# Kernel optimization log

Measured on AMD Instinct MI355X. Metric: run time of the kernel, lower is better.

Reference implementation:

```python
import jax, jax.numpy as jnp
import numpy as np

KS = 3          # kernel_size
DIL = 6         # dilation
PAD = 6         # padding
N = KS * KS     # sampling points per pixel
EPS = 1e-5      # BatchNorm eps


def conv2d(x, w, b=None, padding=0):
    out = jax.lax.conv_general_dilated(
        x, w, window_strides=(1, 1),
        padding=[(padding, padding), (padding, padding)],
        dimension_numbers=('NCHW', 'OIHW', 'NCHW'))
    if b is not None:
        out = out + b[None, :, None, None]
    return out


def setup_inputs() -> dict:
    key = jax.random.key(0)
    ks = jax.random.split(key, 6)
    B, C, H, W, P = 4, 256, 64, 64, 256
    x = jax.random.normal(ks[0], (B, C, H, W), jnp.float32)
    # offset-predicting conv (2N channels), kaiming-ish scale, kept small so offsets are sane
    w_p = jax.random.normal(ks[1], (2 * N, C, 3, 3), jnp.float32) * 0.02
    b_p = jnp.zeros((2 * N,), jnp.float32)
    # modulation-mask conv (N channels)
    w_m = jax.random.normal(ks[2], (N, C, 3, 3), jnp.float32) * 0.02
    b_m = jnp.zeros((N,), jnp.float32)
    # main deform-conv weight (no bias)
    w = jax.random.normal(ks[3], (P, C, KS, KS), jnp.float32) * (2.0 / (C * N)) ** 0.5
    gamma = jnp.ones((P,), jnp.float32)   # BN weight (init fill 1)
    beta = jnp.zeros((P,), jnp.float32)   # BN bias  (init fill 0)
    return dict(x=x, w_p=w_p, b_p=b_p, w_m=w_m, b_m=b_m, w=w, gamma=gamma, beta=beta)


def deform_conv(x, w_p, b_p, w_m, b_m, w):
    B, C, H, W = x.shape
    offset = conv2d(x, w_p, b_p, padding=1)                 # [B, 2N, H, W]
    m = jax.nn.sigmoid(conv2d(x, w_m, b_m, padding=1))      # [B, N, H, W] modulation mask

    x_pad = jnp.pad(x, ((0, 0), (0, 0), (PAD, PAD), (PAD, PAD)))
    Hp, Wp = H + 2 * PAD, W + 2 * PAD

    # p = p_0 (base grid, starts at 1 into padded map) + p_n (dilated kernel grid) + offset
    r = (KS - 1) // 2
    pn = jnp.arange(-r, r + 1, dtype=jnp.float32) * DIL
    pn_x, pn_y = jnp.meshgrid(pn, pn, indexing='ij')        # row-major matches conv weight layout
    p0_x = jnp.arange(1, H + 1, dtype=jnp.float32)
    p0_y = jnp.arange(1, W + 1, dtype=jnp.float32)
    off_x = offset[:, :N].transpose(0, 2, 3, 1)             # [B, H, W, N]
    off_y = offset[:, N:].transpose(0, 2, 3, 1)
    px = p0_x[None, :, None, None] + pn_x.reshape(-1)[None, None, None, :] + off_x
    py = p0_y[None, None, :, None] + pn_y.reshape(-1)[None, None, None, :] + off_y

    q_lt_x = jnp.clip(jnp.floor(px), 0, Hp - 1)
    q_lt_y = jnp.clip(jnp.floor(py), 0, Wp - 1)
    q_rb_x = jnp.clip(jnp.floor(px) + 1, 0, Hp - 1)
    q_rb_y = jnp.clip(jnp.floor(py) + 1, 0, Wp - 1)
    px = jnp.clip(px, 0, Hp - 1)
    py = jnp.clip(py, 0, Wp - 1)

    x_flat = x_pad.reshape(B, C, Hp * Wp)

    def gather(qx, qy):
        idx = (qx * Wp + qy).astype(jnp.int32).reshape(B, 1, -1)   # [B,1,H*W*N]
        v = jnp.take_along_axis(x_flat, jnp.broadcast_to(idx, (B, C, idx.shape[-1])), axis=2)
        return v.reshape(B, C, H, W, N)

    # bilinear weights (deform-conv-v2 formulation)
    g_lt = (1 + (q_lt_x - px)) * (1 + (q_lt_y - py))
    g_rb = (1 - (q_rb_x - px)) * (1 - (q_rb_y - py))
    g_lb = (1 + (q_lt_x - px)) * (1 - (q_rb_y - py))
    g_rt = (1 - (q_rb_x - px)) * (1 + (q_lt_y - py))

    x_off = (g_lt[:, None] * gather(q_lt_x, q_lt_y)
             + g_rb[:, None] * gather(q_rb_x, q_rb_y)
             + g_lb[:, None] * gather(q_lt_x, q_rb_y)
             + g_rt[:, None] * gather(q_rb_x, q_lt_y))     # [B, C, H, W, N]

    x_off = x_off * m.transpose(0, 2, 3, 1)[:, None]        # apply modulation

    # stride-KS conv over the tiled x_offset == einsum over kernel positions
    wk = w.reshape(w.shape[0], C, N)
    return jnp.einsum('bchwk,ock->bohw', x_off, wk)


def reference(x, w_p, b_p, w_m, b_m, w, gamma, beta):
    y = deform_conv(x, w_p, b_p, w_m, b_m, w)
    # BatchNorm2d, training mode (batch stats, biased variance)
    mean = y.mean(axis=(0, 2, 3), keepdims=True)
    var = ((y - mean) ** 2).mean(axis=(0, 2, 3), keepdims=True)
    y = (y - mean) * jax.lax.rsqrt(var + EPS)
    y = y * gamma[None, :, None, None] + beta[None, :, None, None]
    return jax.nn.relu(y)
```

## Files before the change

kernel.cpp:

```cpp
#include <hip/hip_runtime.h>
#include <math.h>

#define CC 256
#define PP 256
#define XSTR 296

#define WS_OFF   0ull
#define WS_Y     442368ull
#define WS_SUM   4636672ull
#define WS_SUMSQ 4636928ull
#define WS_SCALE 4637184ull
#define WS_SHIFT 4637440ull
#define WS_XT    4637696ull
#define WS_WF    6734848ull
#define WS_WPMF  7029760ull

typedef __attribute__((ext_vector_type(8))) short bf16x8;
typedef __attribute__((ext_vector_type(4))) float f32x4;

static __device__ inline unsigned short f2bf(float f) {
  unsigned int u = __float_as_uint(f);
  unsigned int r = (u + 0x7FFFu + ((u >> 16) & 1u)) >> 16;
  return (unsigned short)r;
}
static __device__ inline float bf2f(short s) {
  return __uint_as_float(((unsigned)(unsigned short)s) << 16);
}

__global__ __launch_bounds__(256) void k_prep(const float* __restrict__ x,
                                              const float* __restrict__ w,
                                              const float* __restrict__ w_p,
                                              const float* __restrict__ w_m,
                                              float* __restrict__ ws) {
  int blk = blockIdx.x, t = threadIdx.x;
  if (blk < 1024) {
    __shared__ float sT[64][65];
    int b = blk >> 8, h = (blk >> 2) & 63, c0 = (blk & 3) * 64;
    const float* xs = x + ((size_t)(b * 256 + c0) * 64 + h) * 64;
    int cl = t >> 6, wl = t & 63;
#pragma unroll
    for (int it = 0; it < 16; ++it) {
      int c = cl + it * 4;
      sT[c][wl] = xs[(size_t)c * 4096 + wl];
    }
    __syncthreads();
    unsigned short* xt = (unsigned short*)(ws + WS_XT) +
                         ((size_t)b * 64 + h) * 16384 + c0;
    int c2 = t & 63, w2l = t >> 6;
#pragma unroll
    for (int it = 0; it < 16; ++it) {
      int w2 = w2l + it * 4;
      xt[(size_t)w2 * 256 + c2] = f2bf(sT[c2][w2]);
    }
  } else {
    int gid = (blk - 1024) * 256 + t;
    if (blk == 1024 && t < 512) ws[WS_SUM + t] = 0.f;
    unsigned short* wfb = (unsigned short*)(ws + WS_WF);
    for (int e = gid; e < 589824; e += 163840) {
      int j = e & 7, ocin = (e >> 3) & 15, quad = (e >> 7) & 3;
      int ot = (e >> 9) & 15, ksg = e >> 13;
      int kb = ksg / 9, ks = ksg - kb * 9;
      int c = kb * 32 + quad * 8 + j;
      int oc = ot * 16 + ocin;
      wfb[e] = f2bf(w[((size_t)oc * CC + c) * 9 + ks]);
    }
    unsigned short* wpmf = (unsigned short*)(ws + WS_WPMF);
    for (int e = gid; e < 73728; e += 163840) {
      int j = e & 7, ocin = (e >> 3) & 15, quad = (e >> 7) & 3;
      int ot = (e >> 9) & 1, ksg = e >> 10;
      int kb = ksg / 9, ks = ksg - kb * 9;
      int c = kb * 32 + quad * 8 + j;
      int oc = ot * 16 + ocin;
      float v = 0.f;
      if (oc < 18)      v = w_p[((size_t)oc * CC + c) * 9 + ks];
      else if (oc < 27) v = w_m[((size_t)(oc - 18) * CC + c) * 9 + ks];
      wpmf[e] = f2bf(v);
    }
  }
}

__global__ __launch_bounds__(512, 4) void k_offmask(const float* __restrict__ b_p,
                                                    const float* __restrict__ b_m,
                                                    float* __restrict__ ws) {
  const unsigned short* xT = (const unsigned short*)(ws + WS_XT);
  const unsigned short* wpmf = (const unsigned short*)(ws + WS_WPMF);
  float* offm = ws + WS_OFF;
  __shared__ __align__(16) unsigned short sXo0[32 * XSTR];
  __shared__ __align__(16) unsigned short sXo1[32 * XSTR];

  int t = threadIdx.x, blk = blockIdx.x;
  int xcd = blk & 7, ii = blk >> 3;
  int b = xcd >> 1, h = (xcd & 1) * 32 + (ii >> 1), side = ii & 1;

  int lane = t & 63, wv = __builtin_amdgcn_readfirstlane(t >> 6);
  int pxt = wv & 1, ot = (wv >> 1) & 1, kh = wv >> 2;
  f32x4 acc = {0.f, 0.f, 0.f, 0.f};
  const unsigned short* xb = xT + (size_t)b * 1048576;
  int q = t & 3, uq = t >> 2;

  int oa[3], odst[3];
#pragma unroll
  for (int r = 0; r < 3; ++r) {
    int u = r * 128 + uq;
    odst[r] = -1;
    oa[r] = -1;
    if (u < 288) {
      int j = u >> 5, px = u & 31;
      int row = h + j / 3 - 1, col = side * 32 + px + j % 3 - 1;
      odst[r] = px * XSTR + j * 32 + q * 8;
      if ((unsigned)row < 64u && (unsigned)col < 64u)
        oa[r] = (row * 64 + col) * 256 + q * 8;
    }
  }

  auto stage = [&](int kb, unsigned short* buf) {
    int cb = kb * 32;
#pragma unroll
    for (int r = 0; r < 3; ++r) {
      if (odst[r] >= 0) {
        bf16x8 v = {0, 0, 0, 0, 0, 0, 0, 0};
        if (oa[r] >= 0) v = *(const bf16x8*)(xb + oa[r] + cb);
        *(bf16x8*)&buf[odst[r]] = v;
      }
    }
  };

  stage(0, sXo0);
  __syncthreads();
  for (int kb = 0; kb < 8; ++kb) {
    unsigned short* cur = (kb & 1) ? sXo1 : sXo0;
    unsigned short* nxt = (kb & 1) ? sXo0 : sXo1;
    if (kb < 7) stage(kb + 1, nxt);
    const unsigned short* bb =
        &cur[(pxt * 16 + (lane & 15)) * XSTR + (lane >> 4) * 8];
#pragma unroll
    for (int ks = 0; ks < 9; ++ks) {
      if ((int)(ks >= 5) == kh) {
        int ksg = kb * 9 + ks;
        bf16x8 af =
            *(const bf16x8*)(wpmf + (size_t)ksg * 1024 + ot * 512 + lane * 8);
        bf16x8 bf = *(const bf16x8*)(bb + ks * 32);
        acc = __builtin_amdgcn_mfma_f32_16x16x32_bf16(af, bf, acc, 0, 0, 0);
      }
    }
    __syncthreads();
  }

  float* sR = (float*)sXo0;
  if (kh == 1) {
    int base = (pxt * 2 + ot) * 256 + lane * 4;
#pragma unroll
    for (int r = 0; r < 4; ++r) sR[base + r] = acc[r];
  }
  __syncthreads();
  if (kh == 0) {
    int base = (pxt * 2 + ot) * 256 + lane * 4;
    int pxl = side * 32 + pxt * 16 + (lane & 15);
#pragma unroll
    for (int r = 0; r < 4; ++r) {
      int oc = ot * 16 + (lane >> 4) * 4 + r;
      if (oc < 27) {
        float v = acc[r] + sR[base + r];
        v += (oc < 18) ? b_p[oc] : b_m[oc - 18];
        if (oc >= 18) v = 1.f / (1.f + expf(-v));
        offm[((size_t)b * 27 + oc) * 4096 + h * 64 + pxl] = v;
      }
    }
  }
}

__global__ __launch_bounds__(512, 4) void k_deform(float* __restrict__ ws) {
  const float* offm = ws + WS_OFF;
  const unsigned short* xT = (const unsigned short*)(ws + WS_XT);
  const unsigned short* wfb = (const unsigned short*)(ws + WS_WF);
  float* y = ws + WS_Y;

  __shared__ __align__(16) unsigned short sXu0[32 * XSTR];
  __shared__ __align__(16) unsigned short sXu1[32 * XSTR];

  int t = threadIdx.x, blk = blockIdx.x;
  int xcd = blk & 7, ii = blk >> 3;
  int b = xcd >> 1, h = (xcd & 1) * 32 + (ii >> 1), side = ii & 1;

  int q = t & 3, uq = t >> 2;
  int ta0[3], ta1[3], ta2[3], ta3[3], tdst[3];
  float tg0[3], tg1[3], tg2[3], tg3[3];
#pragma unroll
  for (int r = 0; r < 3; ++r) {
    int u = r * 128 + uq;
    tdst[r] = -1;
    if (u < 288) {
      int k = u >> 5, px = u & 31;
      int w = side * 32 + px;
      size_t base = ((size_t)b * 27) * 4096 + h * 64 + w;
      float offx = offm[base + (size_t)k * 4096];
      float offy = offm[base + (size_t)(9 + k) * 4096];
      float mk   = offm[base + (size_t)(18 + k) * 4096];
      float pnx = (float)((k / 3 - 1) * 6);
      float pny = (float)((k % 3 - 1) * 6);
      float pxf = (float)(h + 1) + pnx + offx;
      float pyf = (float)(w + 1) + pny + offy;
      float fx = floorf(pxf), fy = floorf(pyf);
      float q0x = fminf(fmaxf(fx, 0.f), 75.f);
      float q1x = fminf(fmaxf(fx + 1.f, 0.f), 75.f);
      float q0y = fminf(fmaxf(fy, 0.f), 75.f);
      float q1y = fminf(fmaxf(fy + 1.f, 0.f), 75.f);
      float pxc = fminf(fmaxf(pxf, 0.f), 75.f);
      float pyc = fminf(fmaxf(pyf, 0.f), 75.f);
      float glt = (1.f + (q0x - pxc)) * (1.f + (q0y - pyc));
      float grb = (1.f - (q1x - pxc)) * (1.f - (q1y - pyc));
      float glb = (1.f + (q0x - pxc)) * (1.f - (q1y - pyc));
      float grt = (1.f - (q1x - pxc)) * (1.f + (q0y - pyc));
      int ix0 = (int)q0x - 6, ix1 = (int)q1x - 6;
      int iy0 = (int)q0y - 6, iy1 = (int)q1y - 6;
      bool v00 = (unsigned)ix0 < 64u && (unsigned)iy0 < 64u;
      bool v11 = (unsigned)ix1 < 64u && (unsigned)iy1 < 64u;
      bool v01 = (unsigned)ix0 < 64u && (unsigned)iy1 < 64u;
      bool v10 = (unsigned)ix1 < 64u && (unsigned)iy0 < 64u;
      ta0[r] = (v00 ? (ix0 * 64 + iy0) : 0) * 256 + q * 8;
      ta1[r] = (v11 ? (ix1 * 64 + iy1) : 0) * 256 + q * 8;
      ta2[r] = (v01 ? (ix0 * 64 + iy1) : 0) * 256 + q * 8;
      ta3[r] = (v10 ? (ix1 * 64 + iy0) : 0) * 256 + q * 8;
      tg0[r] = v00 ? glt * mk : 0.f;
      tg1[r] = v11 ? grb * mk : 0.f;
      tg2[r] = v01 ? glb * mk : 0.f;
      tg3[r] = v10 ? grt * mk : 0.f;
      tdst[r] = px * XSTR + k * 32 + q * 8;
    }
  }

  int lane = t & 63, wv = __builtin_amdgcn_readfirstlane(t >> 6);
  f32x4 acc[2][2];
#pragma unroll
  for (int i = 0; i < 2; ++i)
#pragma unroll
    for (int jj = 0; jj < 2; ++jj) acc[i][jj] = (f32x4){0.f, 0.f, 0.f, 0.f};

  const unsigned short* xb = xT + (size_t)b * 1048576;

  auto stage = [&](int kb, unsigned short* buf) {
    int cb = kb * 32;
#pragma unroll
    for (int r = 0; r < 3; ++r) {
      if (tdst[r] >= 0) {
        bf16x8 t0 = *(const bf16x8*)(xb + ta0[r] + cb);
        bf16x8 t1 = *(const bf16x8*)(xb + ta1[r] + cb);
        bf16x8 t2 = *(const bf16x8*)(xb + ta2[r] + cb);
        bf16x8 t3 = *(const bf16x8*)(xb + ta3[r] + cb);
        float g0 = tg0[r], g1 = tg1[r], g2 = tg2[r], g3 = tg3[r];
        unsigned short pk[8];
#pragma unroll
        for (int i = 0; i < 8; ++i) {
          float val = g0 * bf2f(t0[i]);
          val = fmaf(g1, bf2f(t1[i]), val);
          val = fmaf(g2, bf2f(t2[i]), val);
          val = fmaf(g3, bf2f(t3[i]), val);
          pk[i] = f2bf(val);
        }
        uint4 w4;
        w4.x = (unsigned)pk[0] | ((unsigned)pk[1] << 16);
        w4.y = (unsigned)pk[2] | ((unsigned)pk[3] << 16);
        w4.z = (unsigned)pk[4] | ((unsigned)pk[5] << 16);
        w4.w = (unsigned)pk[6] | ((unsigned)pk[7] << 16);
        *(uint4*)&buf[tdst[r]] = w4;
      }
    }
  };

  stage(0, sXu0);
  __syncthreads();
  for (int kb = 0; kb < 8; ++kb) {
    unsigned short* cur = (kb & 1) ? sXu1 : sXu0;
    unsigned short* nxt = (kb & 1) ? sXu0 : sXu1;
    if (kb < 7) stage(kb + 1, nxt);
    const unsigned short* bb0 = &cur[(lane & 15) * XSTR + (lane >> 4) * 8];
    const unsigned short* bb1 = bb0 + 16 * XSTR;
#pragma unroll
    for (int ks = 0; ks < 9; ++ks) {
      int ksg = kb * 9 + ks;
      const unsigned short* ap =
          wfb + (size_t)ksg * 8192 + (size_t)wv * 1024 + lane * 8;
      bf16x8 af0 = *(const bf16x8*)ap;
      bf16x8 af1 = *(const bf16x8*)(ap + 512);
      bf16x8 bf0 = *(const bf16x8*)(bb0 + ks * 32);
      bf16x8 bf1 = *(const bf16x8*)(bb1 + ks * 32);
      acc[0][0] = __builtin_amdgcn_mfma_f32_16x16x32_bf16(af0, bf0, acc[0][0], 0, 0, 0);
      acc[0][1] = __builtin_amdgcn_mfma_f32_16x16x32_bf16(af0, bf1, acc[0][1], 0, 0, 0);
      acc[1][0] = __builtin_amdgcn_mfma_f32_16x16x32_bf16(af1, bf0, acc[1][0], 0, 0, 0);
      acc[1][1] = __builtin_amdgcn_mfma_f32_16x16x32_bf16(af1, bf1, acc[1][1], 0, 0, 0);
    }
    __syncthreads();
  }

  float* sP = (float*)sXu0;
  float* sP2 = sP + 256;
  int quad = lane >> 4, li = lane & 15;
  size_t ybase = ((size_t)b * PP) * 4096 + h * 64 + side * 32;
#pragma unroll
  for (int otl = 0; otl < 2; ++otl) {
#pragma unroll
    for (int r = 0; r < 4; ++r) {
      int oc = wv * 32 + otl * 16 + quad * 4 + r;
      float v0 = acc[otl][0][r];
      float v1 = acc[otl][1][r];
      float* yp = y + ybase + (size_t)oc * 4096 + li;
      yp[0] = v0;
      yp[16] = v1;
      float s = v0 + v1;
      float s2 = fmaf(v0, v0, v1 * v1);
      s += __shfl_xor(s, 1);  s2 += __shfl_xor(s2, 1);
      s += __shfl_xor(s, 2);  s2 += __shfl_xor(s2, 2);
      s += __shfl_xor(s, 4);  s2 += __shfl_xor(s2, 4);
      s += __shfl_xor(s, 8);  s2 += __shfl_xor(s2, 8);
      if (li == 0) {
        sP[oc] = s;
        sP2[oc] = s2;
      }
    }
  }
  __syncthreads();
  if (t < 256) {
    atomicAdd(&ws[WS_SUM + t], sP[t]);
    atomicAdd(&ws[WS_SUMSQ + t], sP2[t]);
  }
}

__global__ void k_stats(float* __restrict__ ws, const float* __restrict__ gamma,
                        const float* __restrict__ beta) {
  int t = threadIdx.x;
  float s  = ws[WS_SUM + t];
  float s2 = ws[WS_SUMSQ + t];
  float mean = s * (1.f / 16384.f);
  float var  = fmaf(s2, 1.f / 16384.f, -mean * mean);
  float rstd = rsqrtf(var + 1e-5f);
  float sc = gamma[t] * rstd;
  ws[WS_SCALE + t] = sc;
  ws[WS_SHIFT + t] = fmaf(-mean, sc, beta[t]);
}

__global__ void k_bnrelu(const float* __restrict__ ws, float* __restrict__ out) {
  const float4* y4 = (const float4*)(ws + WS_Y);
  const float* scale = ws + WS_SCALE;
  const float* shift = ws + WS_SHIFT;
  float4* o4 = (float4*)out;
  const int n4 = 4 * PP * 1024;
  for (int i = blockIdx.x * blockDim.x + threadIdx.x; i < n4;
       i += gridDim.x * blockDim.x) {
    int oc = (i >> 10) & 255;
    float sc = scale[oc], sh = shift[oc];
    float4 v = y4[i];
    float4 r;
    r.x = fmaxf(fmaf(v.x, sc, sh), 0.f);
    r.y = fmaxf(fmaf(v.y, sc, sh), 0.f);
    r.z = fmaxf(fmaf(v.z, sc, sh), 0.f);
    r.w = fmaxf(fmaf(v.w, sc, sh), 0.f);
    o4[i] = r;
  }
}

extern "C" void kernel_launch(void* const* d_in, const int* in_sizes, int n_in,
                              void* d_out, int out_size, void* d_ws,
                              size_t ws_size, hipStream_t stream) {
  const float* x     = (const float*)d_in[0];
  const float* w_p   = (const float*)d_in[1];
  const float* b_p   = (const float*)d_in[2];
  const float* w_m   = (const float*)d_in[3];
  const float* b_m   = (const float*)d_in[4];
  const float* w     = (const float*)d_in[5];
  const float* gamma = (const float*)d_in[6];
  const float* beta  = (const float*)d_in[7];
  float* ws  = (float*)d_ws;
  float* out = (float*)d_out;

  k_prep<<<1664, 256, 0, stream>>>(x, w, w_p, w_m, ws);
  k_offmask<<<512, 512, 0, stream>>>(b_p, b_m, ws);
  k_deform<<<512, 512, 0, stream>>>(ws);
  k_stats<<<1, 256, 0, stream>>>(ws, gamma, beta);
  k_bnrelu<<<2048, 256, 0, stream>>>(ws, out);
}
```

Before: 159.0 us.

## Fuse offset/mask conv into deform kernel, store y as bf16, fold stats into BN

The offset/mask convolution moves into the deform kernel, so each block computes its own 27 channels into shared memory and no longer writes or re-reads a global offset buffer. The stats kernel is removed: the BN+ReLU pass recomputes scale and shift per element from the sums. The intermediate y is stored as bf16 to halve its write and read traffic, at some precision cost. Launch bounds rise to 6 blocks per CU, and bf16 packing now uses the library conversion intrinsic.

```diff
diff --git a/kernel.cpp b/kernel.cpp
--- a/kernel.cpp
+++ b/kernel.cpp
@@ -1,19 +1,17 @@
 #include <hip/hip_runtime.h>
+#include <hip/hip_bf16.h>
 #include <math.h>
 
 #define CC 256
 #define PP 256
 #define XSTR 296
 
-#define WS_OFF   0ull
-#define WS_Y     442368ull
-#define WS_SUM   4636672ull
-#define WS_SUMSQ 4636928ull
-#define WS_SCALE 4637184ull
-#define WS_SHIFT 4637440ull
-#define WS_XT    4637696ull
-#define WS_WF    6734848ull
-#define WS_WPMF  7029760ull
+#define WS_SUM   0ull
+#define WS_SUMSQ 256ull
+#define WS_YU    512ull
+#define WS_XT    2097664ull
+#define WS_WF    4194816ull
+#define WS_WPMF  4489728ull
 
 typedef __attribute__((ext_vector_type(8))) short bf16x8;
 typedef __attribute__((ext_vector_type(4))) float f32x4;
@@ -25,6 +23,11 @@
 }
 static __device__ inline float bf2f(short s) {
   return __uint_as_float(((unsigned)(unsigned short)s) << 16);
+}
+static __device__ inline unsigned pack_bf2(float a, float b) {
+  union { __hip_bfloat162 h2; unsigned u; } cv;
+  cv.h2 = __float22bfloat162_rn(float2{a, b});
+  return cv.u;
 }
 
 __global__ __launch_bounds__(256) void k_prep(const float* __restrict__ x,
@@ -79,110 +82,99 @@
   }
 }
 
-__global__ __launch_bounds__(512, 4) void k_offmask(const float* __restrict__ b_p,
-                                                    const float* __restrict__ b_m,
-                                                    float* __restrict__ ws) {
+__global__ __launch_bounds__(512, 6) void k_deform(const float* __restrict__ b_p,
+                                                   const float* __restrict__ b_m,
+                                                   float* __restrict__ ws) {
   const unsigned short* xT = (const unsigned short*)(ws + WS_XT);
+  const unsigned short* wfb = (const unsigned short*)(ws + WS_WF);
   const unsigned short* wpmf = (const unsigned short*)(ws + WS_WPMF);
-  float* offm = ws + WS_OFF;
-  __shared__ __align__(16) unsigned short sXo0[32 * XSTR];
-  __shared__ __align__(16) unsigned short sXo1[32 * XSTR];
+  unsigned short* y = (unsigned short*)(ws + WS_YU);
+
+  __shared__ __align__(16) unsigned short sXu0[32 * XSTR];
+  __shared__ __align__(16) unsigned short sXu1[32 * XSTR];
+  __shared__ float sOff[27 * 32];
 
   int t = threadIdx.x, blk = blockIdx.x;
   int xcd = blk & 7, ii = blk >> 3;
   int b = xcd >> 1, h = (xcd & 1) * 32 + (ii >> 1), side = ii & 1;
 
   int lane = t & 63, wv = __builtin_amdgcn_readfirstlane(t >> 6);
-  int pxt = wv & 1, ot = (wv >> 1) & 1, kh = wv >> 2;
-  f32x4 acc = {0.f, 0.f, 0.f, 0.f};
+  int q = t & 3, uq = t >> 2;
   const unsigned short* xb = xT + (size_t)b * 1048576;
-  int q = t & 3, uq = t >> 2;
-
-  int oa[3], odst[3];
-#pragma unroll
-  for (int r = 0; r < 3; ++r) {
-    int u = r * 128 + uq;
-    odst[r] = -1;
-    oa[r] = -1;
-    if (u < 288) {
-      int j = u >> 5, px = u & 31;
-      int row = h + j / 3 - 1, col = side * 32 + px + j % 3 - 1;
-      odst[r] = px * XSTR + j * 32 + q * 8;
-      if ((unsigned)row < 64u && (unsigned)col < 64u)
-        oa[r] = (row * 64 + col) * 256 + q * 8;
-    }
-  }
-
-  auto stage = [&](int kb, unsigned short* buf) {
-    int cb = kb * 32;
+
+  {
+    int oa[3], odst[3];
 #pragma unroll
     for (int r = 0; r < 3; ++r) {
-      if (odst[r] >= 0) {
-        bf16x8 v = {0, 0, 0, 0, 0, 0, 0, 0};
-        if (oa[r] >= 0) v = *(const bf16x8*)(xb + oa[r] + cb);
-        *(bf16x8*)&buf[odst[r]] = v;
-      }
-    }
-  };
-
-  stage(0, sXo0);
-  __syncthreads();
-  for (int kb = 0; kb < 8; ++kb) {
-    unsigned short* cur = (kb & 1) ? sXo1 : sXo0;
-    unsigned short* nxt = (kb & 1) ? sXo0 : sXo1;
-    if (kb < 7) stage(kb + 1, nxt);
-    const unsigned short* bb =
-        &cur[(pxt * 16 + (lane & 15)) * XSTR + (lane >> 4) * 8];
-#pragma unroll
-    for (int ks = 0; ks < 9; ++ks) {
-      if ((int)(ks >= 5) == kh) {
-        int ksg = kb * 9 + ks;
-        bf16x8 af =
-            *(const bf16x8*)(wpmf + (size_t)ksg * 1024 + ot * 512 + lane * 8);
-        bf16x8 bf = *(const bf16x8*)(bb + ks * 32);
-        acc = __builtin_amdgcn_mfma_f32_16x16x32_bf16(af, bf, acc, 0, 0, 0);
-      }
-    }
-    __syncthreads();
-  }
-
-  float* sR = (float*)sXo0;
-  if (kh == 1) {
-    int base = (pxt * 2 + ot) * 256 + lane * 4;
-#pragma unroll
-    for (int r = 0; r < 4; ++r) sR[base + r] = acc[r];
-  }
-  __syncthreads();
-  if (kh == 0) {
-    int base = (pxt * 2 + ot) * 256 + lane * 4;
-    int pxl = side * 32 + pxt * 16 + (lane & 15);
-#pragma unroll
-    for (int r = 0; r < 4; ++r) {
-      int oc = ot * 16 + (lane >> 4) * 4 + r;
-      if (oc < 27) {
-        float v = acc[r] + sR[base + r];
-        v += (oc < 18) ? b_p[oc] : b_m[oc - 18];
-        if (oc >= 18) v = 1.f / (1.f + expf(-v));
-        offm[((size_t)b * 27 + oc) * 4096 + h * 64 + pxl] = v;
-      }
-    }
-  }
-}
-
-__global__ __launch_bounds__(512, 4) void k_deform(float* __restrict__ ws) {
-  const float* offm = ws + WS_OFF;
-  const unsigned short* xT = (const unsigned short*)(ws + WS_XT);
-  const unsigned short* wfb = (const unsigned short*)(ws + WS_WF);
-  float* y = ws + WS_Y;
-
-  __shared__ __align__(16) unsigned short sXu0[32 * XSTR];
-  __shared__ __align__(16) unsigned short sXu1[32 * XSTR];
-
-  int t = threadIdx.x, blk = blockIdx.x;
-  int xcd = blk & 7, ii = blk >> 3;
-  int b = xcd >> 1, h = (xcd & 1) * 32 + (ii >> 1), side = ii & 1;
-
-  int q = t & 3, uq = t >> 2;
+      int u = r * 128 + uq;
+      odst[r] = -1;
+      oa[r] = -1;
+      if (u < 288) {
+        int j = u >> 5, px = u & 31;
+        int row = h + j / 3 - 1, col = side * 32 + px + j % 3 - 1;
+        odst[r] = px * XSTR + j * 32 + q * 8;
+        if ((unsigned)row < 64u && (unsigned)col < 64u)
+          oa[r] = (row * 64 + col) * 256 + q * 8;
+      }
+    }
+    auto stage1 = [&](int kb, unsigned short* buf) {
+      int cb = kb * 32;
+#pragma unroll
+      for (int r = 0; r < 3; ++r) {
+        if (odst[r] >= 0) {
+          bf16x8 v = {0, 0, 0, 0, 0, 0, 0, 0};
+          if (oa[r] >= 0) v = *(const bf16x8*)(xb + oa[r] + cb);
+          *(bf16x8*)&buf[odst[r]] = v;
+        }
+      }
+    };
+
+    int pxt = wv & 1, ot = (wv >> 1) & 1, kh = wv >> 2;
+    f32x4 accP = {0.f, 0.f, 0.f, 0.f};
+    stage1(0, sXu0);
+    __syncthreads();
+    for (int kb = 0; kb < 8; ++kb) {
+      unsigned short* cur = (kb & 1) ? sXu1 : sXu0;
+      unsigned short* nxt = (kb & 1) ? sXu0 : sXu1;
+      if (kb < 7) stage1(kb + 1, nxt);
+      const unsigned short* bb =
+          &cur[(pxt * 16 + (lane & 15)) * XSTR + (lane >> 4) * 8];
+#pragma unroll
+      for (int ks = 0; ks < 9; ++ks) {
+        if ((int)(ks >= 5) == kh) {
+          int ksg = kb * 9 + ks;
+          bf16x8 af =
+              *(const bf16x8*)(wpmf + (size_t)ksg * 1024 + ot * 512 + lane * 8);
+          bf16x8 bf = *(const bf16x8*)(bb + ks * 32);
+          accP = __builtin_amdgcn_mfma_f32_16x16x32_bf16(af, bf, accP, 0, 0, 0);
+        }
+      }
+      __syncthreads();
+    }
+    float* sR = (float*)sXu0;
+    if (kh == 1) {
+      int base = (pxt * 2 + ot) * 256 + lane * 4;
+#pragma unroll
+      for (int r = 0; r < 4; ++r) sR[base + r] = accP[r];
+    }
+    __syncthreads();
+    if (kh == 0) {
+      int base = (pxt * 2 + ot) * 256 + lane * 4;
+      int pxl = pxt * 16 + (lane & 15);
+#pragma unroll
+      for (int r = 0; r < 4; ++r) {
+        int oc = ot * 16 + (lane >> 4) * 4 + r;
+        if (oc < 27) {
+          float v = accP[r] + sR[base + r];
+          v += (oc < 18) ? b_p[oc] : b_m[oc - 18];
+          if (oc >= 18) v = 1.f / (1.f + expf(-v));
+          sOff[oc * 32 + pxl] = v;
+        }
+      }
+    }
+    __syncthreads();
+  }
+
   int ta0[3], ta1[3], ta2[3], ta3[3], tdst[3];
   float tg0[3], tg1[3], tg2[3], tg3[3];
 #pragma unroll
@@ -192,10 +184,9 @@
     if (u < 288) {
       int k = u >> 5, px = u & 31;
       int w = side * 32 + px;
-      size_t base = ((size_t)b * 27) * 4096 + h * 64 + w;
-      float offx = offm[base + (size_t)k * 4096];
-      float offy = offm[base + (size_t)(9 + k) * 4096];
-      float mk   = offm[base + (size_t)(18 + k) * 4096];
+      float offx = sOff[k * 32 + px];
+      float offy = sOff[(9 + k) * 32 + px];
+      float mk   = sOff[(18 + k) * 32 + px];
       float pnx = (float)((k / 3 - 1) * 6);
       float pny = (float)((k % 3 - 1) * 6);
       float pxf = (float)(h + 1) + pnx + offx;
@@ -229,16 +220,13 @@
     }
   }
 
-  int lane = t & 63, wv = __builtin_amdgcn_readfirstlane(t >> 6);
   f32x4 acc[2][2];
 #pragma unroll
   for (int i = 0; i < 2; ++i)
 #pragma unroll
     for (int jj = 0; jj < 2; ++jj) acc[i][jj] = (f32x4){0.f, 0.f, 0.f, 0.f};
 
-  const unsigned short* xb = xT + (size_t)b * 1048576;
-
-  auto stage = [&](int kb, unsigned short* buf) {
+  auto stage2 = [&](int kb, unsigned short* buf) {
     int cb = kb * 32;
 #pragma unroll
     for (int r = 0; r < 3; ++r) {
@@ -248,31 +236,31 @@
         bf16x8 t2 = *(const bf16x8*)(xb + ta2[r] + cb);
         bf16x8 t3 = *(const bf16x8*)(xb + ta3[r] + cb);
         float g0 = tg0[r], g1 = tg1[r], g2 = tg2[r], g3 = tg3[r];
-        unsigned short pk[8];
+        float v[8];
 #pragma unroll
         for (int i = 0; i < 8; ++i) {
           float val = g0 * bf2f(t0[i]);
           val = fmaf(g1, bf2f(t1[i]), val);
           val = fmaf(g2, bf2f(t2[i]), val);
           val = fmaf(g3, bf2f(t3[i]), val);
-          pk[i] = f2bf(val);
+          v[i] = val;
         }
         uint4 w4;
-        w4.x = (unsigned)pk[0] | ((unsigned)pk[1] << 16);
-        w4.y = (unsigned)pk[2] | ((unsigned)pk[3] << 16);
-        w4.z = (unsigned)pk[4] | ((unsigned)pk[5] << 16);
-        w4.w = (unsigned)pk[6] | ((unsigned)pk[7] << 16);
+        w4.x = pack_bf2(v[0], v[1]);
+        w4.y = pack_bf2(v[2], v[3]);
+        w4.z = pack_bf2(v[4], v[5]);
+        w4.w = pack_bf2(v[6], v[7]);
         *(uint4*)&buf[tdst[r]] = w4;
       }
     }
   };
 
-  stage(0, sXu0);
+  stage2(0, sXu0);
   __syncthreads();
   for (int kb = 0; kb < 8; ++kb) {
     unsigned short* cur = (kb & 1) ? sXu1 : sXu0;
     unsigned short* nxt = (kb & 1) ? sXu0 : sXu1;
-    if (kb < 7) stage(kb + 1, nxt);
+    if (kb < 7) stage2(kb + 1, nxt);
     const unsigned short* bb0 = &cur[(lane & 15) * XSTR + (lane >> 4) * 8];
     const unsigned short* bb1 = bb0 + 16 * XSTR;
 #pragma unroll
@@ -303,9 +291,9 @@
       int oc = wv * 32 + otl * 16 + quad * 4 + r;
       float v0 = acc[otl][0][r];
       float v1 = acc[otl][1][r];
-      float* yp = y + ybase + (size_t)oc * 4096 + li;
-      yp[0] = v0;
-      yp[16] = v1;
+      unsigned short* yp = y + ybase + (size_t)oc * 4096 + li;
+      yp[0] = f2bf(v0);
+      yp[16] = f2bf(v1);
       float s = v0 + v1;
       float s2 = fmaf(v0, v0, v1 * v1);
       s += __shfl_xor(s, 1);  s2 += __shfl_xor(s2, 1);
@@ -325,36 +313,34 @@
   }
 }
 
-__global__ void k_stats(float* __restrict__ ws, const float* __restrict__ gamma,
-                        const float* __restrict__ beta) {
-  int t = threadIdx.x;
-  float s  = ws[WS_SUM + t];
-  float s2 = ws[WS_SUMSQ + t];
-  float mean = s * (1.f / 16384.f);
-  float var  = fmaf(s2, 1.f / 16384.f, -mean * mean);
-  float rstd = rsqrtf(var + 1e-5f);
-  float sc = gamma[t] * rstd;
-  ws[WS_SCALE + t] = sc;
-  ws[WS_SHIFT + t] = fmaf(-mean, sc, beta[t]);
-}
-
-__global__ void k_bnrelu(const float* __restrict__ ws, float* __restrict__ out) {
-  const float4* y4 = (const float4*)(ws + WS_Y);
-  const float* scale = ws + WS_SCALE;
-  const float* shift = ws + WS_SHIFT;
+__global__ __launch_bounds__(256) void k_bnrelu(const float* __restrict__ ws,
+                                                const float* __restrict__ gamma,
+                                                const float* __restrict__ beta,
+                                                float* __restrict__ out) {
+  const uint4* y8 = (const uint4*)(ws + WS_YU);
   float4* o4 = (float4*)out;
-  const int n4 = 4 * PP * 1024;
-  for (int i = blockIdx.x * blockDim.x + threadIdx.x; i < n4;
+  const int n8 = 4 * PP * 512;
+  for (int i = blockIdx.x * blockDim.x + threadIdx.x; i < n8;
        i += gridDim.x * blockDim.x) {
-    int oc = (i >> 10) & 255;
-    float sc = scale[oc], sh = shift[oc];
-    float4 v = y4[i];
-    float4 r;
-    r.x = fmaxf(fmaf(v.x, sc, sh), 0.f);
-    r.y = fmaxf(fmaf(v.y, sc, sh), 0.f);
-    r.z = fmaxf(fmaf(v.z, sc, sh), 0.f);
-    r.w = fmaxf(fmaf(v.w, sc, sh), 0.f);
-    o4[i] = r;
+    int oc = (i >> 9) & 255;
+    float s = ws[WS_SUM + oc], s2 = ws[WS_SUMSQ + oc];
+    float mean = s * (1.f / 16384.f);
+    float var = fmaf(s2, 1.f / 16384.f, -mean * mean);
+    float rstd = rsqrtf(var + 1e-5f);
+    float sc = gamma[oc] * rstd;
+    float sh = fmaf(-mean, sc, beta[oc]);
+    uint4 v = y8[i];
+    float4 r0, r1;
+    r0.x = fmaxf(fmaf(bf2f((short)(v.x & 0xFFFFu)), sc, sh), 0.f);
+    r0.y = fmaxf(fmaf(bf2f((short)(v.x >> 16)), sc, sh), 0.f);
+    r0.z = fmaxf(fmaf(bf2f((short)(v.y & 0xFFFFu)), sc, sh), 0.f);
+    r0.w = fmaxf(fmaf(bf2f((short)(v.y >> 16)), sc, sh), 0.f);
+    r1.x = fmaxf(fmaf(bf2f((short)(v.z & 0xFFFFu)), sc, sh), 0.f);
+    r1.y = fmaxf(fmaf(bf2f((short)(v.z >> 16)), sc, sh), 0.f);
+    r1.z = fmaxf(fmaf(bf2f((short)(v.w & 0xFFFFu)), sc, sh), 0.f);
+    r1.w = fmaxf(fmaf(bf2f((short)(v.w >> 16)), sc, sh), 0.f);
+    o4[i * 2] = r0;
+    o4[i * 2 + 1] = r1;
   }
 }
 
@@ -373,8 +359,6 @@
   float* out = (float*)d_out;
 
   k_prep<<<1664, 256, 0, stream>>>(x, w, w_p, w_m, ws);
-  k_offmask<<<512, 512, 0, stream>>>(b_p, b_m, ws);
-  k_deform<<<512, 512, 0, stream>>>(ws);
-  k_stats<<<1, 256, 0, stream>>>(ws, gamma, beta);
-  k_bnrelu<<<2048, 256, 0, stream>>>(ws, out);
-}
+  k_deform<<<512, 512, 0, stream>>>(b_p, b_m, ws);
+  k_bnrelu<<<1024, 256, 0, stream>>>(ws, gamma, beta, out);
+}
```

After: 178.2 us. +12.0%, slower.
